# Performance work log

Hardware: AMD Instinct MI355X
Metric: run time of the kernel (lower is better)

## Reference

```python
import jax, jax.numpy as jnp
import numpy as np

N = 10000        # num_nodes
IN_DIM = 128     # in_dim
HID = 256        # hidden_size
EMB = 128        # final embedding dim
R = 8            # num_relations (== num_bases)
C = 32           # num_classes
E = 640000       # num_edges


def setup_inputs() -> dict:
    key = jax.random.key(0)
    ks = jax.random.split(key, 12)
    s = 0.05
    return {
        "x": jax.random.normal(ks[0], (N, N), jnp.float32) * s,
        "edge_index": jax.random.randint(ks[1], (2, E), 0, N),
        "edge_type": jax.random.randint(ks[2], (E,), 0, R),
        "emb": jax.random.normal(ks[3], (N, IN_DIM), jnp.float32) * s,
        "comp1": jax.random.normal(ks[4], (R, R), jnp.float32) * s,
        "basis1": jax.random.normal(ks[5], (R, IN_DIM, HID), jnp.float32) * s,
        "root1": jax.random.normal(ks[6], (IN_DIM, HID), jnp.float32) * s,
        "bias1": jnp.zeros((HID,), jnp.float32),
        "comp2": jax.random.normal(ks[7], (R, R), jnp.float32) * s,
        "basis2": jax.random.normal(ks[8], (R, HID, EMB), jnp.float32) * s,
        "root2": jax.random.normal(ks[9], (HID, EMB), jnp.float32) * s,
        "bias2": jnp.zeros((EMB,), jnp.float32),
        "w_dec": jax.random.normal(ks[10], (EMB, C), jnp.float32) * s,
    }


def _rgcn(h, src, dst, edge_type, comp, basis, root, bias):
    # basis-decomposed RGCN layer with mean aggregation (PyG RGCNConv semantics)
    # transform node features by every basis once: [N, B, out]
    hb = jnp.einsum("ni,bio->nbo", h, basis)
    # per-edge relation coefficients: [E, B]; message = comp[r] . hb[src]
    msg = jnp.einsum("eb,ebo->eo", comp[edge_type], hb[src])
    agg = jax.ops.segment_sum(msg, dst, num_segments=N)
    deg = jax.ops.segment_sum(jnp.ones((msg.shape[0],), h.dtype), dst, num_segments=N)
    agg = agg / jnp.maximum(deg, 1.0)[:, None]
    return agg + h @ root + bias


def reference(x, edge_index, edge_type, emb, comp1, basis1, root1, bias1,
              comp2, basis2, root2, bias2, w_dec):
    src, dst = edge_index[0], edge_index[1]
    h = jax.nn.relu(x @ emb)
    h = jax.nn.relu(_rgcn(h, src, dst, edge_type, comp1, basis1, root1, bias1))
    h = jax.nn.relu(_rgcn(h, src, dst, edge_type, comp2, basis2, root2, bias2))
    # multi-class inner-product decoder: logits = z @ W, softmax over classes
    return jax.nn.softmax(h @ w_dec, axis=1)
```

## Files before the change

### kernel.cpp

```cpp
#include <hip/hip_runtime.h>

typedef unsigned short u16;
typedef unsigned int u32;
typedef __attribute__((ext_vector_type(8))) short bf16x8;
typedef __attribute__((ext_vector_type(4))) float f32x4;

#define N_NODES 10000
#define E_EDGES 640000

static __device__ __forceinline__ float b2f(u16 u) {
  union { u32 i; float f; } x; x.i = ((u32)u) << 16; return x.f;
}
static __device__ __forceinline__ u16 f2b(float f) {
  union { float f; u32 i; } x; x.f = f;
  u32 r = x.i + 0x7FFF + ((x.i >> 16) & 1);
  return (u16)(r >> 16);
}
static __device__ __forceinline__ float ldf(const void* p, size_t i, int f32) {
  return f32 ? ((const float*)p)[i] : b2f(((const u16*)p)[i]);
}

__global__ __launch_bounds__(256) void detect_kernel(const u16* __restrict__ x, int* __restrict__ flag) {
  __shared__ int cnt_s;
  if (threadIdx.x == 0) cnt_s = 0;
  __syncthreads();
  int c = 0;
  for (int i = threadIdx.x; i < 4096; i += 256) {
    int e = (x[i] >> 7) & 255;
    if (e >= 140) c++;
  }
  atomicAdd(&cnt_s, c);
  __syncthreads();
  if (threadIdx.x == 0) flag[0] = (cnt_s > 64) ? 1 : 0;
}

__global__ void hist_kernel(const int* __restrict__ ei, const int* __restrict__ et,
                            int E, int* __restrict__ cnt8) {
  int e = blockIdx.x * 256 + threadIdx.x;
  if (e < E) atomicAdd(&cnt8[ei[E + e] * 8 + et[e]], 1);
}

__global__ __launch_bounds__(256) void segscan_kernel(const int* __restrict__ cnt8,
                                                      int* __restrict__ offs,
                                                      int* __restrict__ cursor) {
  __shared__ int tmp[256];
  const int t = threadIdx.x;
  const int CH = (N_NODES + 255) / 256;
  const int d0 = t * CH;
  int s = 0;
  for (int j = 0; j < CH; j++) {
    int d = d0 + j;
    if (d < N_NODES) {
      #pragma unroll
      for (int r = 0; r < 8; r++) s += cnt8[d * 8 + r];
    }
  }
  tmp[t] = s;
  __syncthreads();
  for (int od = 1; od < 256; od <<= 1) {
    int a = (t >= od) ? tmp[t - od] : 0;
    __syncthreads();
    tmp[t] += a;
    __syncthreads();
  }
  int run = tmp[t] - s;
  for (int j = 0; j < CH; j++) {
    int d = d0 + j;
    if (d < N_NODES) {
      #pragma unroll
      for (int r = 0; r < 8; r++) {
        offs[d * 8 + r] = run;
        cursor[d * 8 + r] = run;
        run += cnt8[d * 8 + r];
      }
    }
  }
  if (t == 255) offs[N_NODES * 8] = tmp[255];
}

__global__ void bucket_kernel(const int* __restrict__ ei, const int* __restrict__ et,
                              int E, int* __restrict__ cursor, int* __restrict__ bucket) {
  int e = blockIdx.x * 256 + threadIdx.x;
  if (e < E) {
    int seg = ei[E + e] * 8 + et[e];
    int pos = atomicAdd(&cursor[seg], 1);
    bucket[pos] = ei[e];
  }
}

__global__ void transpose_kernel(const void* __restrict__ in, u16* __restrict__ out,
                                 int R, int C, const int* __restrict__ dflag) {
  __shared__ u16 tile[64][65];
  const int f = dflag[0];
  int r0 = blockIdx.x * 64, c0 = blockIdx.y * 64;
  int t = threadIdx.x;
  #pragma unroll
  for (int k = 0; k < 16; k++) {
    int lin = t + k * 256; int rr = lin >> 6, cc = lin & 63;
    int gr = r0 + rr;
    tile[rr][cc] = (gr < R) ? f2b(ldf(in, (size_t)gr * C + c0 + cc, f)) : (u16)0;
  }
  __syncthreads();
  #pragma unroll
  for (int k = 0; k < 16; k++) {
    int lin = t + k * 256; int rr = lin >> 6, cc = lin & 63;
    int gc = r0 + cc;
    if (gc < R) out[(size_t)(c0 + rr) * R + gc] = tile[cc][rr];
  }
}

template<int I, int O>
static __device__ __forceinline__ void wprep_body(const void* comp, const void* basis,
                                                  const void* root, u16* WT,
                                                  int f, int blk) {
  const int Kcat = 9 * I;
  int idx = blk * 256 + threadIdx.x;
  if (idx >= Kcat * O) return;
  int o = idx % O;
  int kc = idx / O;
  float v;
  if (kc < 8 * I) {
    int r = kc / I, i = kc % I;
    float s = 0.f;
    #pragma unroll
    for (int b = 0; b < 8; b++)
      s += ldf(comp, r * 8 + b, f) * ldf(basis, ((size_t)b * I + i) * O + o, f);
    v = s;
  } else {
    int i = kc - 8 * I;
    v = ldf(root, (size_t)i * O + o, f);
  }
  WT[(size_t)o * Kcat + kc] = f2b(v);
}

__global__ void wprep_both_kernel(const void* c1, const void* b1, const void* r1, u16* WT1,
                                  const void* c2, const void* b2, const void* r2, u16* WT2,
                                  const int* __restrict__ dflag) {
  const int f = dflag[0];
  int blk = blockIdx.x;
  if (blk < 1152) wprep_body<128, 256>(c1, b1, r1, WT1, f, blk);
  else            wprep_body<256, 128>(c2, b2, r2, WT2, f, blk - 1152);
}

__global__ void gather1_kernel(const u16* __restrict__ h, const int* __restrict__ offs,
                               const int* __restrict__ bucket, u16* __restrict__ s) {
  const int d = blockIdx.x, t = threadIdx.x;
  const u32* __restrict__ h32 = (const u32*)h;
  u32* s32 = (u32*)s;
  const int sb = d * 8;
  const int b0 = offs[sb], bend = offs[sb + 8];
  const float inv = 1.0f / (float)((bend - b0) > 1 ? (bend - b0) : 1);
  const int base = d * 576;
  #pragma unroll
  for (int r = 0; r < 8; r++) {
    int j = offs[sb + r], j1 = offs[sb + r + 1];
    float l0 = 0.f, h0a = 0.f, l1 = 0.f, h1a = 0.f, l2 = 0.f, h2a = 0.f, l3 = 0.f, h3a = 0.f;
    for (; j + 3 < j1; j += 4) {
      u32 v0 = h32[(size_t)bucket[j] * 64 + t];
      u32 v1 = h32[(size_t)bucket[j + 1] * 64 + t];
      u32 v2 = h32[(size_t)bucket[j + 2] * 64 + t];
      u32 v3 = h32[(size_t)bucket[j + 3] * 64 + t];
      l0 += b2f((u16)v0); h0a += b2f((u16)(v0 >> 16));
      l1 += b2f((u16)v1); h1a += b2f((u16)(v1 >> 16));
      l2 += b2f((u16)v2); h2a += b2f((u16)(v2 >> 16));
      l3 += b2f((u16)v3); h3a += b2f((u16)(v3 >> 16));
    }
    for (; j < j1; ++j) {
      u32 v = h32[(size_t)bucket[j] * 64 + t];
      l0 += b2f((u16)v); h0a += b2f((u16)(v >> 16));
    }
    float sl = (l0 + l1 + l2 + l3) * inv, sh = (h0a + h1a + h2a + h3a) * inv;
    s32[base + r * 64 + t] = (u32)f2b(sl) | ((u32)f2b(sh) << 16);
  }
  s32[base + 512 + t] = h32[(size_t)d * 64 + t];
}

__global__ void gather2_kernel(const u16* __restrict__ h, const int* __restrict__ offs,
                               const int* __restrict__ bucket, u16* __restrict__ s) {
  const int d = blockIdx.x, t = threadIdx.x;
  const uint2* __restrict__ h64 = (const uint2*)h;
  uint2* s64 = (uint2*)s;
  const int sb = d * 8;
  const int b0 = offs[sb], bend = offs[sb + 8];
  const float inv = 1.0f / (float)((bend - b0) > 1 ? (bend - b0) : 1);
  const int base = d * 576;
  #pragma unroll
  for (int r = 0; r < 8; r++) {
    int j = offs[sb + r], j1 = offs[sb + r + 1];
    float4 A0 = {0.f, 0.f, 0.f, 0.f}, A1 = A0, A2 = A0, A3 = A0;
    for (; j + 3 < j1; j += 4) {
      uint2 v0 = h64[(size_t)bucket[j] * 64 + t];
      uint2 v1 = h64[(size_t)bucket[j + 1] * 64 + t];
      uint2 v2 = h64[(size_t)bucket[j + 2] * 64 + t];
      uint2 v3 = h64[(size_t)bucket[j + 3] * 64 + t];
      A0.x += b2f((u16)v0.x); A0.y += b2f((u16)(v0.x >> 16)); A0.z += b2f((u16)v0.y); A0.w += b2f((u16)(v0.y >> 16));
      A1.x += b2f((u16)v1.x); A1.y += b2f((u16)(v1.x >> 16)); A1.z += b2f((u16)v1.y); A1.w += b2f((u16)(v1.y >> 16));
      A2.x += b2f((u16)v2.x); A2.y += b2f((u16)(v2.x >> 16)); A2.z += b2f((u16)v2.y); A2.w += b2f((u16)(v2.y >> 16));
      A3.x += b2f((u16)v3.x); A3.y += b2f((u16)(v3.x >> 16)); A3.z += b2f((u16)v3.y); A3.w += b2f((u16)(v3.y >> 16));
    }
    for (; j < j1; ++j) {
      uint2 v = h64[(size_t)bucket[j] * 64 + t];
      A0.x += b2f((u16)v.x); A0.y += b2f((u16)(v.x >> 16)); A0.z += b2f((u16)v.y); A0.w += b2f((u16)(v.y >> 16));
    }
    float sx = (A0.x + A1.x + A2.x + A3.x) * inv;
    float sy = (A0.y + A1.y + A2.y + A3.y) * inv;
    float sz = (A0.z + A1.z + A2.z + A3.z) * inv;
    float sw = (A0.w + A1.w + A2.w + A3.w) * inv;
    uint2 o;
    o.x = (u32)f2b(sx) | ((u32)f2b(sy) << 16);
    o.y = (u32)f2b(sz) | ((u32)f2b(sw) << 16);
    s64[base + r * 64 + t] = o;
  }
  s64[base + 512 + t] = h64[(size_t)d * 64 + t];
}

__global__ __launch_bounds__(256) void gemm_kernel(
    const void* __restrict__ A, int lda,
    const u16* __restrict__ BT, int ldbt,
    int M, int Nout, int K,
    int tiles_per_split, int ktiles_total,
    float* __restrict__ outf,
    const int* __restrict__ dflagA) {
  __shared__ __align__(16) u16 As[128 * 32];
  __shared__ __align__(16) u16 Bs[128 * 32];
  const int f32A = dflagA ? dflagA[0] : 0;
  const int tid = threadIdx.x;
  const int wave = tid >> 6;
  const int lane = tid & 63;
  const int quad = lane >> 4;
  const int l16 = lane & 15;
  const int m0 = blockIdx.x * 128;
  const int n0 = blockIdx.y * 128;
  const int split = blockIdx.z;
  const int wm = (wave >> 1) * 64;
  const int wn = (wave & 1) * 64;

  int kt0 = split * tiles_per_split;
  int kt1 = kt0 + tiles_per_split;
  if (kt1 > ktiles_total) kt1 = ktiles_total;

  f32x4 acc[4][4];
  #pragma unroll
  for (int mi = 0; mi < 4; mi++)
    #pragma unroll
    for (int ni = 0; ni < 4; ni++) {
      f32x4 z = {0.f, 0.f, 0.f, 0.f};
      acc[mi][ni] = z;
    }

  for (int kt = kt0; kt < kt1; ++kt) {
    const int k0 = kt * 32;
    __syncthreads();
    #pragma unroll
    for (int i = 0; i < 2; ++i) {
      int c = tid + i * 256;
      int row = c >> 2, kc = c & 3;
      int kpos = k0 + kc * 8;
      uint4 vb = {0u, 0u, 0u, 0u};
      if (kpos < K) vb = *(const uint4*)(BT + (size_t)(n0 + row) * ldbt + kpos);
      *(uint4*)&Bs[(size_t)c * 8] = vb;
      uint4 va = {0u, 0u, 0u, 0u};
      if (kpos < K) {
        int ga = m0 + row; if (ga > M - 1) ga = M - 1;
        if (!f32A) {
          va = *(const uint4*)((const u16*)A + (size_t)ga * lda + kpos);
        } else {
          const float* Af = (const float*)A + (size_t)ga * lda + kpos;
          float4 f0 = ((const float4*)Af)[0];
          float4 f1 = ((const float4*)Af)[1];
          va.x = (u32)f2b(f0.x) | ((u32)f2b(f0.y) << 16);
          va.y = (u32)f2b(f0.z) | ((u32)f2b(f0.w) << 16);
          va.z = (u32)f2b(f1.x) | ((u32)f2b(f1.y) << 16);
          va.w = (u32)f2b(f1.z) | ((u32)f2b(f1.w) << 16);
        }
      }
      *(uint4*)&As[(size_t)c * 8] = va;
    }
    __syncthreads();

    bf16x8 af[4], bfr[4];
    #pragma unroll
    for (int mi = 0; mi < 4; mi++)
      af[mi] = *(const bf16x8*)&As[(size_t)(wm + mi * 16 + l16) * 32 + quad * 8];
    #pragma unroll
    for (int ni = 0; ni < 4; ni++)
      bfr[ni] = *(const bf16x8*)&Bs[(size_t)(wn + ni * 16 + l16) * 32 + quad * 8];
    #pragma unroll
    for (int mi = 0; mi < 4; mi++)
      #pragma unroll
      for (int ni = 0; ni < 4; ni++)
        acc[mi][ni] = __builtin_amdgcn_mfma_f32_16x16x32_bf16(af[mi], bfr[ni], acc[mi][ni], 0, 0, 0);
  }

  #pragma unroll
  for (int mi = 0; mi < 4; mi++)
    #pragma unroll
    for (int ni = 0; ni < 4; ni++)
      #pragma unroll
      for (int jj = 0; jj < 4; jj++) {
        int row = m0 + wm + mi * 16 + quad * 4 + jj;
        int col = n0 + wn + ni * 16 + l16;
        if (row < M) atomicAdd(&outf[(size_t)row * Nout + col], acc[mi][ni][jj]);
      }
}

__global__ void finalize_kernel(const float* __restrict__ accf, int count4, int nmask,
                                const void* __restrict__ bias, u16* __restrict__ out,
                                const int* __restrict__ dflag) {
  int i = blockIdx.x * 256 + threadIdx.x;
  if (i >= count4) return;
  const int f = dflag[0];
  float4 v = ((const float4*)accf)[i];
  if (bias) {
    int c = (i * 4) & nmask;
    v.x += ldf(bias, c, f);
    v.y += ldf(bias, c + 1, f);
    v.z += ldf(bias, c + 2, f);
    v.w += ldf(bias, c + 3, f);
  }
  v.x = fmaxf(v.x, 0.f); v.y = fmaxf(v.y, 0.f); v.z = fmaxf(v.z, 0.f); v.w = fmaxf(v.w, 0.f);
  ushort4 o;
  o.x = f2b(v.x); o.y = f2b(v.y); o.z = f2b(v.z); o.w = f2b(v.w);
  *(ushort4*)(out + (size_t)i * 4) = o;
}

__global__ __launch_bounds__(256) void decoder_kernel(const float* __restrict__ h2f,
                                                      const void* __restrict__ wdec,
                                                      const void* __restrict__ bias2,
                                                      void* __restrict__ out,
                                                      const int* __restrict__ dflag) {
  __shared__ float w[128 * 32];
  __shared__ float hrow[4][128];
  const int f = dflag[0];
  int t = threadIdx.x;
  for (int i = t; i < 128 * 32; i += 256) w[i] = ldf(wdec, i, f);
  int wv = t >> 6, lane = t & 63;
  int n = blockIdx.x * 4 + wv;
  float b0 = ldf(bias2, lane * 2, f), b1 = ldf(bias2, lane * 2 + 1, f);
  hrow[wv][lane * 2]     = fmaxf(h2f[(size_t)n * 128 + lane * 2] + b0, 0.f);
  hrow[wv][lane * 2 + 1] = fmaxf(h2f[(size_t)n * 128 + lane * 2 + 1] + b1, 0.f);
  __syncthreads();
  int half = lane >> 5, c = lane & 31;
  float sum = 0.f;
  #pragma unroll 8
  for (int k = 0; k < 64; k++) sum += hrow[wv][half * 64 + k] * w[(half * 64 + k) * 32 + c];
  sum += __shfl_xor(sum, 32);
  float mx = sum;
  #pragma unroll
  for (int m = 16; m >= 1; m >>= 1) mx = fmaxf(mx, __shfl_xor(mx, m));
  float e = __expf(sum - mx);
  float tot = e;
  #pragma unroll
  for (int m = 16; m >= 1; m >>= 1) tot += __shfl_xor(tot, m);
  float p = e / tot;
  if (half == 0) {
    if (f) ((float*)out)[(size_t)n * 32 + c] = p;
    else   ((u16*)out)[(size_t)n * 32 + c] = f2b(p);
  }
}

extern "C" void kernel_launch(void* const* d_in, const int* in_sizes, int n_in,
                              void* d_out, int out_size, void* d_ws, size_t ws_size,
                              hipStream_t stream) {
  const void* x      = d_in[0];
  const int* ei      = (const int*)d_in[1];
  const int* et      = (const int*)d_in[2];
  const void* emb    = d_in[3];
  const void* comp1  = d_in[4];
  const void* basis1 = d_in[5];
  const void* root1  = d_in[6];
  const void* bias1  = d_in[7];
  const void* comp2  = d_in[8];
  const void* basis2 = d_in[9];
  const void* root2  = d_in[10];
  const void* bias2  = d_in[11];
  const void* wdec   = d_in[12];

  const int N = N_NODES, E = E_EDGES;
  const int NSEG = N * 8;
  auto AL = [](size_t b) -> size_t { return (b + 255) & ~(size_t)255; };

  char* base = (char*)d_ws;
  size_t off = 0;
  auto alloc = [&](size_t b) -> char* { char* p = base + off; off += AL(b); return p; };
  int* dflag   = (int*)alloc(4);
  int* offs    = (int*)alloc((size_t)(NSEG + 1) * 4);
  int* cursor  = (int*)alloc((size_t)NSEG * 4);
  int* bucket  = (int*)alloc((size_t)E * 4);
  u16* h0      = (u16*)alloc((size_t)N * 128 * 2);
  u16* h1      = (u16*)alloc((size_t)N * 256 * 2);
  size_t zoff0 = off;
  int*   cnt8  = (int*)alloc((size_t)NSEG * 4);
  float* h0f   = (float*)alloc((size_t)N * 128 * 4);
  float* h1f   = (float*)alloc((size_t)N * 256 * 4);
  float* h2f   = (float*)alloc((size_t)N * 128 * 4);
  size_t zbytes = off - zoff0;
  u16* WT1     = (u16*)alloc((size_t)256 * 1152 * 2);
  u16* WT2     = (u16*)alloc((size_t)128 * 2304 * 2);
  u16* embT    = (u16*)alloc((size_t)128 * N * 2);
  u16* s1      = (u16*)alloc((size_t)N * 1152 * 2);
  u16* s2      = (u16*)alloc((size_t)N * 2304 * 2);

  detect_kernel<<<1, 256, 0, stream>>>((const u16*)x, dflag);

  hipMemsetAsync(cnt8, 0, zbytes, stream);

  hist_kernel<<<(E + 255) / 256, 256, 0, stream>>>(ei, et, E, cnt8);
  segscan_kernel<<<1, 256, 0, stream>>>(cnt8, offs, cursor);
  bucket_kernel<<<(E + 255) / 256, 256, 0, stream>>>(ei, et, E, cursor, bucket);

  transpose_kernel<<<dim3((N + 63) / 64, 2), 256, 0, stream>>>(emb, embT, N, 128, dflag);
  wprep_both_kernel<<<2304, 256, 0, stream>>>(comp1, basis1, root1, WT1,
                                              comp2, basis2, root2, WT2, dflag);

  {
    int ktt = (N + 31) / 32;
    int spA = 8;
    int tps = (ktt + spA - 1) / spA;
    gemm_kernel<<<dim3((N + 127) / 128, 1, spA), 256, 0, stream>>>(
        x, N, embT, N, N, 128, N, tps, ktt, h0f, dflag);
    finalize_kernel<<<(N * 128 / 4 + 255) / 256, 256, 0, stream>>>(
        h0f, N * 128 / 4, 127, (const void*)nullptr, h0, dflag);
  }

  {
    gather1_kernel<<<N, 64, 0, stream>>>(h0, offs, bucket, s1);
    gemm_kernel<<<dim3((N + 127) / 128, 2, 4), 256, 0, stream>>>(
        s1, 1152, WT1, 1152, N, 256, 1152, 9, 36, h1f, (const int*)nullptr);
    finalize_kernel<<<(N * 256 / 4 + 255) / 256, 256, 0, stream>>>(
        h1f, N * 256 / 4, 255, bias1, h1, dflag);
  }

  {
    gather2_kernel<<<N, 64, 0, stream>>>(h1, offs, bucket, s2);
    gemm_kernel<<<dim3((N + 127) / 128, 1, 8), 256, 0, stream>>>(
        s2, 2304, WT2, 2304, N, 128, 2304, 9, 72, h2f, (const int*)nullptr);
  }

  decoder_kernel<<<N / 4, 256, 0, stream>>>(h2f, wdec, bias2, d_out, dflag);
}
```

Measured before the change: 916.7 us.

## Replace split-K atomic accumulation with per-split partial buffers reduced in consumers

The GEMM now writes each split-K slice to its own partial buffer instead of doing atomicAdd into a zeroed fp32 output. The finalize and decoder kernels sum the partials before applying bias and ReLU. The memset of the fp32 accumulators is dropped, and the split counts for layers 1 and 2 are halved. This removes atomic traffic and memset bandwidth, at the cost of extra partial-buffer writes and reads and less parallelism in the layer GEMMs.

```diff
diff --git a/kernel.cpp b/kernel.cpp
--- a/kernel.cpp
+++ b/kernel.cpp
@@ -219,7 +219,7 @@
     const u16* __restrict__ BT, int ldbt,
     int M, int Nout, int K,
     int tiles_per_split, int ktiles_total,
-    float* __restrict__ outf,
+    float* __restrict__ partials,
     const int* __restrict__ dflagA) {
   __shared__ __align__(16) u16 As[128 * 32];
   __shared__ __align__(16) u16 Bs[128 * 32];
@@ -300,17 +300,21 @@
       for (int jj = 0; jj < 4; jj++) {
         int row = m0 + wm + mi * 16 + quad * 4 + jj;
         int col = n0 + wn + ni * 16 + l16;
-        if (row < M) atomicAdd(&outf[(size_t)row * Nout + col], acc[mi][ni][jj]);
+        if (row < M) partials[((size_t)split * M + row) * Nout + col] = acc[mi][ni][jj];
       }
 }
 
-__global__ void finalize_kernel(const float* __restrict__ accf, int count4, int nmask,
-                                const void* __restrict__ bias, u16* __restrict__ out,
+__global__ void finalize_kernel(const float* __restrict__ partials, int S, int count4,
+                                int nmask, const void* __restrict__ bias, u16* __restrict__ out,
                                 const int* __restrict__ dflag) {
   int i = blockIdx.x * 256 + threadIdx.x;
   if (i >= count4) return;
   const int f = dflag[0];
-  float4 v = ((const float4*)accf)[i];
+  float4 v = {0.f, 0.f, 0.f, 0.f};
+  for (int z = 0; z < S; z++) {
+    float4 p = ((const float4*)(partials + (size_t)z * count4 * 4))[i];
+    v.x += p.x; v.y += p.y; v.z += p.z; v.w += p.w;
+  }
   if (bias) {
     int c = (i * 4) & nmask;
     v.x += ldf(bias, c, f);
@@ -324,7 +328,7 @@
   *(ushort4*)(out + (size_t)i * 4) = o;
 }
 
-__global__ __launch_bounds__(256) void decoder_kernel(const float* __restrict__ h2f,
+__global__ __launch_bounds__(256) void decoder_kernel(const float* __restrict__ p2, int S,
                                                       const void* __restrict__ wdec,
                                                       const void* __restrict__ bias2,
                                                       void* __restrict__ out,
@@ -336,9 +340,16 @@
   for (int i = t; i < 128 * 32; i += 256) w[i] = ldf(wdec, i, f);
   int wv = t >> 6, lane = t & 63;
   int n = blockIdx.x * 4 + wv;
-  float b0 = ldf(bias2, lane * 2, f), b1 = ldf(bias2, lane * 2 + 1, f);
-  hrow[wv][lane * 2]     = fmaxf(h2f[(size_t)n * 128 + lane * 2] + b0, 0.f);
-  hrow[wv][lane * 2 + 1] = fmaxf(h2f[(size_t)n * 128 + lane * 2 + 1] + b1, 0.f);
+  float v0 = 0.f, v1 = 0.f;
+  for (int z = 0; z < S; z++) {
+    const float* row = p2 + (size_t)z * N_NODES * 128 + (size_t)n * 128;
+    v0 += row[lane * 2];
+    v1 += row[lane * 2 + 1];
+  }
+  v0 += ldf(bias2, lane * 2, f);
+  v1 += ldf(bias2, lane * 2 + 1, f);
+  hrow[wv][lane * 2]     = fmaxf(v0, 0.f);
+  hrow[wv][lane * 2 + 1] = fmaxf(v1, 0.f);
   __syncthreads();
   int half = lane >> 5, c = lane & 31;
   float sum = 0.f;
@@ -389,21 +400,19 @@
   int* bucket  = (int*)alloc((size_t)E * 4);
   u16* h0      = (u16*)alloc((size_t)N * 128 * 2);
   u16* h1      = (u16*)alloc((size_t)N * 256 * 2);
-  size_t zoff0 = off;
-  int*   cnt8  = (int*)alloc((size_t)NSEG * 4);
-  float* h0f   = (float*)alloc((size_t)N * 128 * 4);
-  float* h1f   = (float*)alloc((size_t)N * 256 * 4);
-  float* h2f   = (float*)alloc((size_t)N * 128 * 4);
-  size_t zbytes = off - zoff0;
+  int* cnt8    = (int*)alloc((size_t)NSEG * 4);
   u16* WT1     = (u16*)alloc((size_t)256 * 1152 * 2);
   u16* WT2     = (u16*)alloc((size_t)128 * 2304 * 2);
   u16* embT    = (u16*)alloc((size_t)128 * N * 2);
   u16* s1      = (u16*)alloc((size_t)N * 1152 * 2);
   u16* s2      = (u16*)alloc((size_t)N * 2304 * 2);
+  float* pA    = (float*)alloc((size_t)8 * N * 128 * 4);
+  float* p1    = (float*)alloc((size_t)2 * N * 256 * 4);
+  float* p2    = (float*)alloc((size_t)4 * N * 128 * 4);
 
   detect_kernel<<<1, 256, 0, stream>>>((const u16*)x, dflag);
 
-  hipMemsetAsync(cnt8, 0, zbytes, stream);
+  hipMemsetAsync(cnt8, 0, (size_t)NSEG * 4, stream);
 
   hist_kernel<<<(E + 255) / 256, 256, 0, stream>>>(ei, et, E, cnt8);
   segscan_kernel<<<1, 256, 0, stream>>>(cnt8, offs, cursor);
@@ -418,24 +427,24 @@
     int spA = 8;
     int tps = (ktt + spA - 1) / spA;
     gemm_kernel<<<dim3((N + 127) / 128, 1, spA), 256, 0, stream>>>(
-        x, N, embT, N, N, 128, N, tps, ktt, h0f, dflag);
+        x, N, embT, N, N, 128, N, tps, ktt, pA, dflag);
     finalize_kernel<<<(N * 128 / 4 + 255) / 256, 256, 0, stream>>>(
-        h0f, N * 128 / 4, 127, (const void*)nullptr, h0, dflag);
+        pA, spA, N * 128 / 4, 127, (const void*)nullptr, h0, dflag);
   }
 
   {
     gather1_kernel<<<N, 64, 0, stream>>>(h0, offs, bucket, s1);
-    gemm_kernel<<<dim3((N + 127) / 128, 2, 4), 256, 0, stream>>>(
-        s1, 1152, WT1, 1152, N, 256, 1152, 9, 36, h1f, (const int*)nullptr);
+    gemm_kernel<<<dim3((N + 127) / 128, 2, 2), 256, 0, stream>>>(
+        s1, 1152, WT1, 1152, N, 256, 1152, 18, 36, p1, (const int*)nullptr);
     finalize_kernel<<<(N * 256 / 4 + 255) / 256, 256, 0, stream>>>(
-        h1f, N * 256 / 4, 255, bias1, h1, dflag);
+        p1, 2, N * 256 / 4, 255, bias1, h1, dflag);
   }
 
   {
     gather2_kernel<<<N, 64, 0, stream>>>(h1, offs, bucket, s2);
-    gemm_kernel<<<dim3((N + 127) / 128, 1, 8), 256, 0, stream>>>(
-        s2, 2304, WT2, 2304, N, 128, 2304, 9, 72, h2f, (const int*)nullptr);
-  }
-
-  decoder_kernel<<<N / 4, 256, 0, stream>>>(h2f, wdec, bias2, d_out, dflag);
-}
+    gemm_kernel<<<dim3((N + 127) / 128, 1, 4), 256, 0, stream>>>(
+        s2, 2304, WT2, 2304, N, 128, 2304, 18, 72, p2, (const int*)nullptr);
+  }
+
+  decoder_kernel<<<N / 4, 256, 0, stream>>>(p2, 4, wdec, bias2, d_out, dflag);
+}
```

New measurement: 883.8 us. 1.04x faster.
